# Performance work log

Measured on AMD Instinct MI355X. Metric: run time of the kernel, lower is better.

The kernel has to match this reference:

```python
import jax, jax.numpy as jnp
import numpy as np

A, B, I, J, K = 8, 256, 256, 256, 256  # a=batch, b=tokens, i=s-channels, j=c-channels, k=out_dim


def setup_inputs() -> dict:
    key = jax.random.key(0)
    k1, k2, k3 = jax.random.split(key, 3)
    input_s = jax.random.normal(k1, (A, B, I), dtype=jnp.float32)
    input_c = jax.random.normal(k2, (B, J), dtype=jnp.float32)
    # learned params: w ~ N(0, 0.02), b zeros (as in build())
    w = jax.random.normal(k3, (I, J, K), dtype=jnp.float32) * 0.02
    b = jnp.zeros((K,), dtype=jnp.float32)
    return {"input_s": input_s, "input_c": input_c, "w": w, "b": b}


def reference(input_s, input_c, w, b):
    # Original: tmp = einsum('abi,ijk->abjk', input_s, w); out = einsum('bj,abjk->abk', input_c, tmp) + b
    # Mathematically identical fused bilinear contraction (avoids the [a,b,j,k] intermediate):
    out = jnp.einsum('abi,bj,ijk->abk', input_s, input_c, w)
    return out + b
```

## Files before the change

### kernel.cpp

```cpp
#include <hip/hip_runtime.h>
#include <hip/hip_bf16.h>

#define A_ 8
#define B_ 256
#define I_ 256
#define J_ 256
#define K_ 256

typedef __attribute__((ext_vector_type(8))) short short8_t;
typedef __attribute__((ext_vector_type(4))) float f32x4_t;
typedef __attribute__((ext_vector_type(4))) uint u32x4_t;

static __device__ __forceinline__ uint pack2bf(float a, float b) {
  float2 f2; f2.x = a; f2.y = b;
  __hip_bfloat162 h2 = __float22bfloat162_rn(f2);
  uint r;
  __builtin_memcpy(&r, &h2, 4);
  return r;
}

static __device__ __forceinline__ ushort f2bf(float f) {
  __hip_bfloat16 h = __float2bfloat16(f);
  ushort us;
  __builtin_memcpy(&us, &h, 2);
  return us;
}

static __device__ __forceinline__ float bf2f(ushort h) {
  uint u = ((uint)h) << 16;
  float f;
  __builtin_memcpy(&f, &u, 4);
  return f;
}

__global__ __launch_bounds__(256) void prepass_kernel(
    const float* __restrict__ c, ushort* __restrict__ cbf) {
  const int idx = blockIdx.x * 256 + threadIdx.x;
  const f32x4_t v = *reinterpret_cast<const f32x4_t*>(c + (size_t)idx * 4);
  uint2 r;
  r.x = pack2bf(v[0], v[1]);
  r.y = pack2bf(v[2], v[3]);
  *reinterpret_cast<uint2*>(cbf + (size_t)idx * 4) = r;
}

#define BK 32
#define LDH 40

__global__ __launch_bounds__(512, 2) void pass1_kernel(
    const ushort* __restrict__ cbf, const float* __restrict__ w,
    ushort* __restrict__ u) {
  const int i    = blockIdx.x;
  const int tid  = threadIdx.x;
  const int lane = tid & 63;
  const int wave = tid >> 6;
  const int wr   = wave >> 2;
  const int wc   = wave & 3;
  const int lrow = lane & 15;
  const int lhi  = lane >> 4;

  __shared__ ushort As[2][256][LDH];
  __shared__ ushort Bt[2][256][LDH];

  const float* wi = w + (size_t)i * (J_ * K_);

  f32x4_t acc[8][4];
#pragma unroll
  for (int m = 0; m < 8; m++)
#pragma unroll
    for (int n = 0; n < 4; n++) acc[m][n] = (f32x4_t)(0.0f);

  const int ar = tid >> 1;
  const int aj = (tid & 1) * 16;
  const int bk = tid & 255;
  const int bj = (tid >> 8) * 16;

  short8_t a8[2];
  float brg[16];

  auto LOAD = [&](int j0) {
    const ushort* sa = cbf + (size_t)ar * J_ + j0 + aj;
    a8[0] = *reinterpret_cast<const short8_t*>(sa);
    a8[1] = *reinterpret_cast<const short8_t*>(sa + 8);
    const float* sb = wi + (size_t)(j0 + bj) * K_ + bk;
#pragma unroll
    for (int q = 0; q < 16; q++) brg[q] = sb[(size_t)q * K_];
  };

  auto STORE = [&](int buf) {
    *reinterpret_cast<short8_t*>(&As[buf][ar][aj])     = a8[0];
    *reinterpret_cast<short8_t*>(&As[buf][ar][aj + 8]) = a8[1];
    u32x4_t t0, t1;
#pragma unroll
    for (int q = 0; q < 4; q++) t0[q] = pack2bf(brg[2 * q], brg[2 * q + 1]);
#pragma unroll
    for (int q = 0; q < 4; q++) t1[q] = pack2bf(brg[8 + 2 * q], brg[9 + 2 * q]);
    *reinterpret_cast<u32x4_t*>(&Bt[buf][bk][bj])     = t0;
    *reinterpret_cast<u32x4_t*>(&Bt[buf][bk][bj + 8]) = t1;
  };

  LOAD(0);
  STORE(0);
  __syncthreads();

  for (int t = 0; t < 8; ++t) {
    if (t < 7) LOAD((t + 1) * BK);
    const int buf = t & 1;
    short8_t afr[8], bfr[4];
#pragma unroll
    for (int m = 0; m < 8; m++)
      afr[m] = *reinterpret_cast<const short8_t*>(
          &As[buf][wr * 128 + m * 16 + lrow][lhi * 8]);
#pragma unroll
    for (int n = 0; n < 4; n++)
      bfr[n] = *reinterpret_cast<const short8_t*>(
          &Bt[buf][wc * 64 + n * 16 + lrow][lhi * 8]);
#pragma unroll
    for (int m = 0; m < 8; m++)
#pragma unroll
      for (int n = 0; n < 4; n++)
        acc[m][n] = __builtin_amdgcn_mfma_f32_16x16x32_bf16(afr[m], bfr[n],
                                                            acc[m][n], 0, 0, 0);
    if (t < 7) STORE(buf ^ 1);
    __syncthreads();
  }

#pragma unroll
  for (int m = 0; m < 8; m++) {
    const int brow = wr * 128 + m * 16 + lhi * 4;
#pragma unroll
    for (int n = 0; n < 4; n++) {
      const int kc = wc * 64 + n * 16 + lrow;
      ushort* up = u + ((size_t)brow * I_ + i) * K_ + kc;
#pragma unroll
      for (int r = 0; r < 4; r++)
        up[(size_t)r * (I_ * K_)] = f2bf(acc[m][n][r]);
    }
  }
}

__global__ __launch_bounds__(256) void pass2_kernel(
    const float* __restrict__ s, const ushort* __restrict__ u,
    const float* __restrict__ bias, float* __restrict__ out) {
  const int b   = blockIdx.x;
  const int a0  = blockIdx.y * 4;
  const int tid = threadIdx.x;
  __shared__ float s_l[4][I_];
  __shared__ float red[8][4][K_];

#pragma unroll
  for (int v = 0; v < 4; v++) {
    const int idx = tid + v * 256;
    const int a = idx >> 8, ii = idx & 255;
    s_l[a][ii] = s[((size_t)(a0 + a) * B_ + b) * I_ + ii];
  }
  __syncthreads();

  const int kb = (tid & 31) * 8;
  const int ig = tid >> 5;
  float acc[4][8];
#pragma unroll
  for (int a = 0; a < 4; a++)
#pragma unroll
    for (int q = 0; q < 8; q++) acc[a][q] = 0.0f;

  const ushort* ub = u + ((size_t)b * I_ + ig * 32) * K_ + kb;
  for (int ii = 0; ii < 32; ++ii) {
    const short8_t uv = *reinterpret_cast<const short8_t*>(ub + (size_t)ii * K_);
    float f[8];
#pragma unroll
    for (int q = 0; q < 8; q++) f[q] = bf2f((ushort)uv[q]);
    const int i = ig * 32 + ii;
#pragma unroll
    for (int a = 0; a < 4; a++) {
      const float sa = s_l[a][i];
#pragma unroll
      for (int q = 0; q < 8; q++) acc[a][q] += sa * f[q];
    }
  }

#pragma unroll
  for (int a = 0; a < 4; a++) {
    f32x4_t r0, r1;
#pragma unroll
    for (int q = 0; q < 4; q++) { r0[q] = acc[a][q]; r1[q] = acc[a][4 + q]; }
    *reinterpret_cast<f32x4_t*>(&red[ig][a][kb])     = r0;
    *reinterpret_cast<f32x4_t*>(&red[ig][a][kb + 4]) = r1;
  }
  __syncthreads();

#pragma unroll
  for (int v = 0; v < 4; v++) {
    const int k = tid;
    float sum = 0.0f;
#pragma unroll
    for (int g = 0; g < 8; g++) sum += red[g][v][k];
    out[((size_t)(a0 + v) * B_ + b) * K_ + k] = sum + bias[k];
  }
}

__global__ __launch_bounds__(256) void fallback_kernel(
    const float* __restrict__ s, const float* __restrict__ cmat,
    const float* __restrict__ w, const float* __restrict__ bias,
    float* __restrict__ out) {
  const int b = blockIdx.x;
  const int k = threadIdx.x;
  __shared__ float c_l[J_];
  __shared__ float s_l[A_][I_];
  for (int idx = threadIdx.x; idx < J_; idx += 256) c_l[idx] = cmat[(size_t)b * J_ + idx];
  for (int idx = threadIdx.x; idx < A_ * I_; idx += 256) {
    const int a = idx >> 8;
    const int i = idx & 255;
    s_l[a][i] = s[(size_t)a * (B_ * I_) + (size_t)b * I_ + i];
  }
  __syncthreads();
  float acc[A_];
#pragma unroll
  for (int a = 0; a < A_; a++) acc[a] = 0.0f;
  for (int i = 0; i < I_; i++) {
    const float* wrow = w + (size_t)i * (J_ * K_) + k;
    float inner = 0.0f;
    for (int j = 0; j < J_; j++) inner += c_l[j] * wrow[(size_t)j * K_];
#pragma unroll
    for (int a = 0; a < A_; a++) acc[a] += s_l[a][i] * inner;
  }
#pragma unroll
  for (int a = 0; a < A_; a++)
    out[((size_t)a * B_ + b) * K_ + k] = acc[a] + bias[k];
}

extern "C" void kernel_launch(void* const* d_in, const int* in_sizes, int n_in,
                              void* d_out, int out_size, void* d_ws, size_t ws_size,
                              hipStream_t stream) {
  const float* s    = (const float*)d_in[0];
  const float* cmat = (const float*)d_in[1];
  const float* w    = (const float*)d_in[2];
  const float* bias = (const float*)d_in[3];
  float* out = (float*)d_out;

  const size_t u_elems = (size_t)B_ * I_ * K_;
  const size_t need = u_elems * sizeof(ushort) + (size_t)B_ * J_ * sizeof(ushort);
  if (ws_size >= need) {
    ushort* u   = (ushort*)d_ws;
    ushort* cbf = (ushort*)d_ws + u_elems;
    prepass_kernel<<<dim3((B_ * J_) / (256 * 4)), dim3(256), 0, stream>>>(cmat, cbf);
    pass1_kernel<<<dim3(I_), dim3(512), 0, stream>>>(cbf, w, u);
    pass2_kernel<<<dim3(B_, 2), dim3(256), 0, stream>>>(s, u, bias, out);
  } else {
    fallback_kernel<<<dim3(B_), dim3(256), 0, stream>>>(s, cmat, w, bias, out);
  }
}
```

Before: 46.10 us.

## Split pass1 over K into four 64-wide blocks and load A fragments directly

Pass1 now launches I x 4 blocks of 256 threads, each computing a 256x64 output tile instead of one 512-thread block computing the full 256x256 tile. This gives 1024 blocks, where before there were only 256 for the machine's many CUs. The A operand (bf16 c) is no longer staged in shared memory. Each wave loads its MFMA fragments straight from global memory into registers, double-buffered, which cuts LDS use and one set of barriers' worth of traffic. The cost is that c is re-read four times across the K-blocks, and the global fragment loads are uncoalesced strided 16-byte reads.

Measured after the change: 42.24 us. -8.4%, faster.

```diff
diff --git a/kernel.cpp b/kernel.cpp
--- a/kernel.cpp
+++ b/kernel.cpp
@@ -44,98 +44,100 @@
 }
 
 #define BK 32
-#define LDH 40
-
-__global__ __launch_bounds__(512, 2) void pass1_kernel(
+#define LDB 40
+
+__global__ __launch_bounds__(256, 2) void pass1_kernel(
     const ushort* __restrict__ cbf, const float* __restrict__ w,
     ushort* __restrict__ u) {
   const int i    = blockIdx.x;
+  const int k0   = blockIdx.y * 64;
   const int tid  = threadIdx.x;
   const int lane = tid & 63;
   const int wave = tid >> 6;
-  const int wr   = wave >> 2;
-  const int wc   = wave & 3;
   const int lrow = lane & 15;
   const int lhi  = lane >> 4;
 
-  __shared__ ushort As[2][256][LDH];
-  __shared__ ushort Bt[2][256][LDH];
-
-  const float* wi = w + (size_t)i * (J_ * K_);
-
-  f32x4_t acc[8][4];
-#pragma unroll
-  for (int m = 0; m < 8; m++)
+  __shared__ ushort Bt[2][64][LDB];
+
+  const float* wi = w + (size_t)i * (J_ * K_) + k0;
+
+  const int bk = tid & 63;
+  const int jb = (tid >> 6) * 8;
+
+  const int arow = wave * 64 + lrow;
+
+  f32x4_t acc[4][4];
+#pragma unroll
+  for (int m = 0; m < 4; m++)
 #pragma unroll
     for (int n = 0; n < 4; n++) acc[m][n] = (f32x4_t)(0.0f);
 
-  const int ar = tid >> 1;
-  const int aj = (tid & 1) * 16;
-  const int bk = tid & 255;
-  const int bj = (tid >> 8) * 16;
-
-  short8_t a8[2];
-  float brg[16];
-
-  auto LOAD = [&](int j0) {
-    const ushort* sa = cbf + (size_t)ar * J_ + j0 + aj;
-    a8[0] = *reinterpret_cast<const short8_t*>(sa);
-    a8[1] = *reinterpret_cast<const short8_t*>(sa + 8);
-    const float* sb = wi + (size_t)(j0 + bj) * K_ + bk;
-#pragma unroll
-    for (int q = 0; q < 16; q++) brg[q] = sb[(size_t)q * K_];
-  };
-
-  auto STORE = [&](int buf) {
-    *reinterpret_cast<short8_t*>(&As[buf][ar][aj])     = a8[0];
-    *reinterpret_cast<short8_t*>(&As[buf][ar][aj + 8]) = a8[1];
-    u32x4_t t0, t1;
-#pragma unroll
-    for (int q = 0; q < 4; q++) t0[q] = pack2bf(brg[2 * q], brg[2 * q + 1]);
-#pragma unroll
-    for (int q = 0; q < 4; q++) t1[q] = pack2bf(brg[8 + 2 * q], brg[9 + 2 * q]);
-    *reinterpret_cast<u32x4_t*>(&Bt[buf][bk][bj])     = t0;
-    *reinterpret_cast<u32x4_t*>(&Bt[buf][bk][bj + 8]) = t1;
-  };
-
-  LOAD(0);
-  STORE(0);
-  __syncthreads();
-
+  float    brg[2][8];
+  short8_t afr[2][4];
+
+#define LOADB(p, j0)                                                       \
+  {                                                                        \
+    const float* sb = wi + (size_t)((j0) + jb) * K_ + bk;                  \
+    _Pragma("unroll") for (int q = 0; q < 8; q++)                          \
+        brg[p][q] = sb[(size_t)q * K_];                                    \
+  }
+#define LOADA(p, j0)                                                       \
+  {                                                                        \
+    _Pragma("unroll") for (int m = 0; m < 4; m++)                          \
+        afr[p][m] = *reinterpret_cast<const short8_t*>(                    \
+            cbf + (size_t)(arow + m * 16) * J_ + (j0) + lhi * 8);          \
+  }
+#define STOREB(buf, p)                                                     \
+  {                                                                        \
+    u32x4_t t4;                                                            \
+    _Pragma("unroll") for (int q = 0; q < 4; q++)                          \
+        t4[q] = pack2bf(brg[p][2 * q], brg[p][2 * q + 1]);                 \
+    *reinterpret_cast<u32x4_t*>(&Bt[buf][bk][jb]) = t4;                    \
+  }
+
+  LOADB(0, 0);
+  LOADA(0, 0);
+  STOREB(0, 0);
+  __syncthreads();
+
+#pragma unroll
   for (int t = 0; t < 8; ++t) {
-    if (t < 7) LOAD((t + 1) * BK);
-    const int buf = t & 1;
-    short8_t afr[8], bfr[4];
-#pragma unroll
-    for (int m = 0; m < 8; m++)
-      afr[m] = *reinterpret_cast<const short8_t*>(
-          &As[buf][wr * 128 + m * 16 + lrow][lhi * 8]);
+    const int cur = t & 1;
+    const int nxt = cur ^ 1;
+    if (t < 7) {
+      LOADB(nxt, (t + 1) * BK);
+      LOADA(nxt, (t + 1) * BK);
+    }
+    short8_t bfr[4];
 #pragma unroll
     for (int n = 0; n < 4; n++)
       bfr[n] = *reinterpret_cast<const short8_t*>(
-          &Bt[buf][wc * 64 + n * 16 + lrow][lhi * 8]);
-#pragma unroll
-    for (int m = 0; m < 8; m++)
+          &Bt[cur][n * 16 + lrow][lhi * 8]);
+#pragma unroll
+    for (int m = 0; m < 4; m++)
 #pragma unroll
       for (int n = 0; n < 4; n++)
-        acc[m][n] = __builtin_amdgcn_mfma_f32_16x16x32_bf16(afr[m], bfr[n],
-                                                            acc[m][n], 0, 0, 0);
-    if (t < 7) STORE(buf ^ 1);
+        acc[m][n] = __builtin_amdgcn_mfma_f32_16x16x32_bf16(
+            afr[cur][m], bfr[n], acc[m][n], 0, 0, 0);
+    if (t < 7) STOREB(nxt, nxt);
     __syncthreads();
   }
 
 #pragma unroll
-  for (int m = 0; m < 8; m++) {
-    const int brow = wr * 128 + m * 16 + lhi * 4;
+  for (int m = 0; m < 4; m++) {
+    const int brow = wave * 64 + m * 16 + lhi * 4;
 #pragma unroll
     for (int n = 0; n < 4; n++) {
-      const int kc = wc * 64 + n * 16 + lrow;
+      const int kc = k0 + n * 16 + lrow;
       ushort* up = u + ((size_t)brow * I_ + i) * K_ + kc;
 #pragma unroll
       for (int r = 0; r < 4; r++)
         up[(size_t)r * (I_ * K_)] = f2bf(acc[m][n][r]);
     }
   }
+#undef LOADB
+#undef LOADA
+#undef STOREB
 }
 
 __global__ __launch_bounds__(256) void pass2_kernel(
@@ -243,7 +245,7 @@
     ushort* u   = (ushort*)d_ws;
     ushort* cbf = (ushort*)d_ws + u_elems;
     prepass_kernel<<<dim3((B_ * J_) / (256 * 4)), dim3(256), 0, stream>>>(cmat, cbf);
-    pass1_kernel<<<dim3(I_), dim3(512), 0, stream>>>(cbf, w, u);
+    pass1_kernel<<<dim3(I_, 4), dim3(256), 0, stream>>>(cbf, w, u);
     pass2_kernel<<<dim3(B_, 2), dim3(256), 0, stream>>>(s, u, bias, out);
   } else {
     fallback_kernel<<<dim3(B_), dim3(256), 0, stream>>>(s, cmat, w, bias, out);
```
